# Optimization experiments

Hardware: AMD Instinct MI355X
Metric: run time of the kernel (lower is better)

The kernel has to match this reference:

```python
import jax, jax.numpy as jnp
import numpy as np

B, H, L, DK = 16, 16, 2048, 64   # batch, heads, query len, head dim
LK = 4096                        # original key length
C = 10                           # num_clusters
LKS = 2 * int(np.log(LK))        # shrunk key length = 16


def _lin(x, w, b):
    # torch nn.Linear: y = x @ W^T + b
    return jnp.matmul(x, w.T) + b


def setup_inputs() -> dict:
    key = jax.random.key(0)
    ks = jax.random.split(key, 20)
    s = 0.05
    inp = {
        "Q": jax.random.normal(ks[0], (B, H, L, DK), jnp.float32),
        "K": jax.random.normal(ks[1], (B, H, LK, DK), jnp.float32),
        "V": jax.random.normal(ks[2], (B, H, LK, DK), jnp.float32),
        # shrink_k / shrink_v: Linear(l_k, 2*log(l_k))
        "shrink_k_w": jax.random.normal(ks[3], (LKS, LK), jnp.float32) * s,
        "shrink_k_b": jax.random.normal(ks[4], (LKS,), jnp.float32) * s,
        "shrink_v_w": jax.random.normal(ks[5], (LKS, LK), jnp.float32) * s,
        "shrink_v_b": jax.random.normal(ks[6], (LKS,), jnp.float32) * s,
        # proj_to_cluster_k: Linear(batch_size, num_clusters) + ReLU
        "proj_w": jax.random.normal(ks[7], (C, B), jnp.float32) * s,
        "proj_b": jax.random.normal(ks[8], (C,), jnp.float32) * s,
        "ck_w": jax.random.normal(ks[9], (C, C), jnp.float32) * s,
        "ck_b": jax.random.normal(ks[10], (C,), jnp.float32) * s,
        "cq_w": jax.random.normal(ks[11], (C, C), jnp.float32) * s,
        "cq_b": jax.random.normal(ks[12], (C,), jnp.float32) * s,
        "mu_w": jax.random.normal(ks[13], (C, C), jnp.float32) * s,
        "mu_b": jax.random.normal(ks[14], (C,), jnp.float32) * s,
        "sig_w": jax.random.normal(ks[15], (C, C), jnp.float32) * s,
        "sig_b": jax.random.normal(ks[16], (C,), jnp.float32) * s,
    }
    return inp


def reference(Q, K, V, shrink_k_w, shrink_k_b, shrink_v_w, shrink_v_b,
              proj_w, proj_b, ck_w, ck_b, cq_w, cq_b, mu_w, mu_b, sig_w, sig_b):
    b = Q.shape[0]
    # shrink along key sequence dim: (b,h,lk,d) -> (b,h,LKS,d)
    Ks = jnp.einsum('bhkd,sk->bhsd', K, shrink_k_w) + shrink_k_b[:, None]
    Vs = jnp.einsum('bhkd,sk->bhsd', V, shrink_v_w) + shrink_v_b[:, None]

    # pad + unfold over the batch dim: window j of K_padded[w:w+b]
    K_padded = jnp.concatenate([jnp.zeros_like(Ks), Ks[1:]], axis=0)  # (2b-1,h,LKS,d)
    idx = jnp.arange(b)[:, None] + jnp.arange(b)[None, :]             # (b, b)
    K_unfold = jnp.moveaxis(K_padded[idx], 1, -1)                     # (b,h,LKS,d,b)

    cluster_k_p = jax.nn.relu(_lin(K_unfold, proj_w, proj_b))         # (b,h,LKS,d,C)
    cluster_k = jax.nn.softmax(_lin(cluster_k_p, ck_w, ck_b), axis=-1)
    cluster_q = jax.nn.softmax(_lin(cluster_k_p, cq_w, cq_b), axis=-1)

    mu = _lin(cluster_q, mu_w, mu_b)
    sigma = jax.nn.softplus(_lin(cluster_q, sig_w, sig_b))
    # Normal log_prob
    log_prob = (-0.5 * jnp.square((cluster_k - mu) / sigma)
                - jnp.log(sigma) - 0.5 * jnp.log(2.0 * jnp.pi).astype(cluster_k.dtype))
    # torch CrossEntropyLoss with probability targets: class dim = dim 1 (= h)
    logp = jax.nn.log_softmax(cluster_q, axis=1)
    ce = -jnp.mean(jnp.sum(cluster_q * logp, axis=1))
    loss = -jnp.mean(log_prob) + ce

    # per-cluster masked mean over the last dim, vectorized over clusters.
    # where(argmax==i, cluster_q, 0).mean(-1) == onehot(argmax)[...,i] * mean(cluster_q,-1)
    masks = jax.nn.one_hot(jnp.argmax(cluster_q, axis=-1), C, dtype=cluster_q.dtype)  # (b,h,LKS,d,C)
    q_mean = jnp.mean(cluster_q, axis=-1)                                              # (b,h,LKS,d)
    q_sub = masks * q_mean[..., None]                                                  # (b,h,LKS,d,C)

    scores = jnp.einsum('bhqd,bhkdc->cbhqk', Q, q_sub)  # (C,b,h,l,LKS)
    final_score = jnp.max(scores, axis=0)               # (b,h,l,LKS)
    attn = jax.nn.softmax(final_score, axis=-1)
    context = jnp.einsum('bhqk,bhkd->bhqd', attn, Vs)   # (b,h,l,d)
    return context, loss
```

## Files before the change

### kernel.cpp

```cpp
#include <hip/hip_runtime.h>

#define KS_OFF 0
#define VS_OFF 262144
#define QM_OFF 524288
#define AM_OFF 786432
#define LP_OFF 1048576
#define CE_OFF 1048832

typedef __attribute__((ext_vector_type(8))) short short8;
typedef __attribute__((ext_vector_type(4))) float f32x4;

__device__ inline unsigned short bfb(float x) {
  unsigned u = __float_as_uint(x);
  return (unsigned short)((u + 0x7fffu + ((u >> 16) & 1u)) >> 16);
}
__device__ inline unsigned pk2(float a, float b) {
  return (unsigned)bfb(a) | ((unsigned)bfb(b) << 16);
}
__device__ inline float bft(unsigned short h) {
  return __uint_as_float((unsigned)h << 16);
}
__device__ inline void split3(float x, unsigned short& h, unsigned short& m, unsigned short& l) {
  unsigned u = __float_as_uint(x);
  h = (unsigned short)(u >> 16);
  float r = x - bft(h);
  m = (unsigned short)(__float_as_uint(r) >> 16);
  float r2 = r - bft(m);
  l = bfb(r2);
}

__global__ __launch_bounds__(256) void k_shrink3(
    const float* __restrict__ K, const float* __restrict__ V,
    const float* __restrict__ skw, const float* __restrict__ skb,
    const float* __restrict__ svw, const float* __restrict__ svb,
    float* __restrict__ ws)
{
  int blk = blockIdx.x;
  int tensor = blk >> 8;
  int bh = blk & 255;
  const float* __restrict__ src = (tensor ? V : K) + (size_t)bh * (4096 * 64);
  const float* __restrict__ w    = tensor ? svw : skw;
  const float* __restrict__ bias = tensor ? svb : skb;
  float* __restrict__ dst = ws + (tensor ? VS_OFF : KS_OFF) + bh * 1024;

  int t = threadIdx.x;
  int wv = t >> 6;
  int l = t & 63;
  int l15 = l & 15;
  int kg = l >> 4;
  union Frag { unsigned u[4]; short8 s8; };

  f32x4 acc[4];
#pragma unroll
  for (int nt = 0; nt < 4; ++nt) acc[nt] = (f32x4){0.f, 0.f, 0.f, 0.f};

  const float* __restrict__ wrow = w + l15 * 4096 + kg * 8;

  int kk0 = wv * 32;
  for (int kk = kk0; kk < kk0 + 32; ++kk) {
    const float* __restrict__ wp = wrow + kk * 32;
    float4 wa = *(const float4*)wp;
    float4 wb = *(const float4*)(wp + 4);
    float we[8] = {wa.x, wa.y, wa.z, wa.w, wb.x, wb.y, wb.z, wb.w};
    Frag ah, am, al;
#pragma unroll
    for (int e = 0; e < 4; ++e) {
      unsigned short h0, m0, l0, h1, m1, l1;
      split3(we[2 * e], h0, m0, l0);
      split3(we[2 * e + 1], h1, m1, l1);
      ah.u[e] = (unsigned)h0 | ((unsigned)h1 << 16);
      am.u[e] = (unsigned)m0 | ((unsigned)m1 << 16);
      al.u[e] = (unsigned)l0 | ((unsigned)l1 << 16);
    }

    int kbase = kk * 32 + kg * 8;
    const float* __restrict__ bp = src + (size_t)kbase * 64 + l15;
#pragma unroll
    for (int nt = 0; nt < 4; ++nt) {
      float v[8];
#pragma unroll
      for (int j = 0; j < 8; ++j) v[j] = bp[j * 64 + nt * 16];
      Frag bh, bm, bl;
#pragma unroll
      for (int e = 0; e < 4; ++e) {
        unsigned short h0, m0, l0, h1, m1, l1;
        split3(v[2 * e], h0, m0, l0);
        split3(v[2 * e + 1], h1, m1, l1);
        bh.u[e] = (unsigned)h0 | ((unsigned)h1 << 16);
        bm.u[e] = (unsigned)m0 | ((unsigned)m1 << 16);
        bl.u[e] = (unsigned)l0 | ((unsigned)l1 << 16);
      }
      acc[nt] = __builtin_amdgcn_mfma_f32_16x16x32_bf16(ah.s8, bh.s8, acc[nt], 0, 0, 0);
      acc[nt] = __builtin_amdgcn_mfma_f32_16x16x32_bf16(ah.s8, bm.s8, acc[nt], 0, 0, 0);
      acc[nt] = __builtin_amdgcn_mfma_f32_16x16x32_bf16(am.s8, bh.s8, acc[nt], 0, 0, 0);
      acc[nt] = __builtin_amdgcn_mfma_f32_16x16x32_bf16(ah.s8, bl.s8, acc[nt], 0, 0, 0);
      acc[nt] = __builtin_amdgcn_mfma_f32_16x16x32_bf16(al.s8, bh.s8, acc[nt], 0, 0, 0);
      acc[nt] = __builtin_amdgcn_mfma_f32_16x16x32_bf16(am.s8, bm.s8, acc[nt], 0, 0, 0);
    }
  }

  __shared__ float red[4][1024];
  int g4 = kg * 4;
#pragma unroll
  for (int nt = 0; nt < 4; ++nt)
#pragma unroll
    for (int r = 0; r < 4; ++r)
      red[wv][(g4 + r) * 64 + nt * 16 + l15] = acc[nt][r];
  __syncthreads();
  for (int p = t; p < 1024; p += 256) {
    int s = p >> 6;
    dst[p] = red[0][p] + red[1][p] + red[2][p] + red[3][p] + bias[s];
  }
}

__global__ __launch_bounds__(1024) void k_cluster(
    const float* __restrict__ pw, const float* __restrict__ pb,
    const float* __restrict__ ckw, const float* __restrict__ ckb,
    const float* __restrict__ cqw, const float* __restrict__ cqb,
    const float* __restrict__ muw, const float* __restrict__ mub,
    const float* __restrict__ sgw, const float* __restrict__ sgb,
    float* __restrict__ ws)
{
  int bidx = blockIdx.x >> 4;
  int sIdx = blockIdx.x & 15;
  int t = threadIdx.x;
  int h = t >> 6, d = t & 63;

  __shared__ float wgt[610];
  __shared__ float cqs[16 * 64 * 10];
  if (t < 160) wgt[t] = pw[t];
  else if (t < 170) wgt[t] = pb[t - 160];
  else if (t < 270) wgt[t] = ckw[t - 170];
  else if (t < 280) wgt[t] = ckb[t - 270];
  else if (t < 380) wgt[t] = cqw[t - 280];
  else if (t < 390) wgt[t] = cqb[t - 380];
  else if (t < 490) wgt[t] = muw[t - 390];
  else if (t < 500) wgt[t] = mub[t - 490];
  else if (t < 600) wgt[t] = sgw[t - 500];
  else if (t < 610) wgt[t] = sgb[t - 600];
  __syncthreads();

  const float* __restrict__ Ks = ws + KS_OFF;

  float ckp[10];
#pragma unroll
  for (int c = 0; c < 10; ++c) ckp[c] = wgt[160 + c];
  for (int m = 1; m <= bidx; ++m) {
    float kv = Ks[((m * 16 + h) * 16 + sIdx) * 64 + d];
    int j = m + 15 - bidx;
#pragma unroll
    for (int c = 0; c < 10; ++c) ckp[c] = fmaf(kv, wgt[c * 16 + j], ckp[c]);
  }
#pragma unroll
  for (int c = 0; c < 10; ++c) ckp[c] = fmaxf(ckp[c], 0.f);

  float zk[10], zq[10];
#pragma unroll
  for (int c = 0; c < 10; ++c) { zk[c] = wgt[270 + c]; zq[c] = wgt[380 + c]; }
#pragma unroll
  for (int j = 0; j < 10; ++j) {
    float v = ckp[j];
#pragma unroll
    for (int c = 0; c < 10; ++c) {
      zk[c] = fmaf(v, wgt[170 + c * 10 + j], zk[c]);
      zq[c] = fmaf(v, wgt[280 + c * 10 + j], zq[c]);
    }
  }
  float mk = zk[0], mq = zq[0];
#pragma unroll
  for (int c = 1; c < 10; ++c) { mk = fmaxf(mk, zk[c]); mq = fmaxf(mq, zq[c]); }
  float sk = 0.f, sq = 0.f;
#pragma unroll
  for (int c = 0; c < 10; ++c) {
    zk[c] = expf(zk[c] - mk); sk += zk[c];
    zq[c] = expf(zq[c] - mq); sq += zq[c];
  }
  float rik = 1.f / sk, riq = 1.f / sq;
#pragma unroll
  for (int c = 0; c < 10; ++c) { zk[c] *= rik; zq[c] *= riq; }

  float mu[10], sgz[10];
#pragma unroll
  for (int c = 0; c < 10; ++c) { mu[c] = wgt[490 + c]; sgz[c] = wgt[600 + c]; }
#pragma unroll
  for (int j = 0; j < 10; ++j) {
    float v = zq[j];
#pragma unroll
    for (int c = 0; c < 10; ++c) {
      mu[c]  = fmaf(v, wgt[390 + c * 10 + j], mu[c]);
      sgz[c] = fmaf(v, wgt[500 + c * 10 + j], sgz[c]);
    }
  }
  float lp = 0.f, qmean = 0.f, best = zq[0];
  int amax = 0;
#pragma unroll
  for (int c = 0; c < 10; ++c) {
    float x = sgz[c];
    float sg = (x > 20.f) ? x : log1pf(expf(x));
    float zr = (zk[c] - mu[c]) / sg;
    lp += -0.5f * zr * zr - logf(sg);
    qmean += zq[c];
    if (c > 0 && zq[c] > best) { best = zq[c]; amax = c; }
  }
  lp -= 10.f * 0.91893853320467274f;
  qmean *= 0.1f;

  int pos = ((bidx * 16 + h) * 16 + sIdx) * 64 + d;
  ws[QM_OFF + pos] = qmean;
  ((int*)ws)[AM_OFF + pos] = amax;
#pragma unroll
  for (int c = 0; c < 10; ++c) cqs[(h * 64 + d) * 10 + c] = zq[c];
  __syncthreads();

  float ce = 0.f;
  if (t < 640) {
    int dd = t / 10, cc = t - dd * 10;
    float x[16];
#pragma unroll
    for (int hh = 0; hh < 16; ++hh) x[hh] = cqs[(hh * 64 + dd) * 10 + cc];
    float mx = x[0];
#pragma unroll
    for (int hh = 1; hh < 16; ++hh) mx = fmaxf(mx, x[hh]);
    float sum = 0.f;
#pragma unroll
    for (int hh = 0; hh < 16; ++hh) sum += expf(x[hh] - mx);
    float lse = mx + logf(sum);
#pragma unroll
    for (int hh = 0; hh < 16; ++hh) ce += x[hh] * (x[hh] - lse);
  }

#pragma unroll
  for (int o = 1; o < 64; o <<= 1) { lp += __shfl_xor(lp, o); ce += __shfl_xor(ce, o); }
  __shared__ float redw[16][2];
  if ((t & 63) == 0) { redw[t >> 6][0] = lp; redw[t >> 6][1] = ce; }
  __syncthreads();
  if (t == 0) {
    float Ls = 0.f, Cs = 0.f;
#pragma unroll
    for (int i = 0; i < 16; ++i) { Ls += redw[i][0]; Cs += redw[i][1]; }
    ws[LP_OFF + blockIdx.x] = Ls;
    ws[CE_OFF + blockIdx.x] = Cs;
  }
}

__global__ __launch_bounds__(512, 4) void k_attn(
    const float* __restrict__ Q, float* __restrict__ out,
    const float* __restrict__ ws)
{
  int bid = blockIdx.x;
  int bh = bid >> 1;
  int half = bid & 1;
  int t = threadIdx.x;
  int wv = t >> 6;
  int l = t & 63;
  int l15 = l & 15;
  int sbase = (l >> 4) * 8;
  int g4 = (l >> 4) * 4;

  __shared__ unsigned short Gm[10][16][72];
  __shared__ float Vs_l[1024];
  __shared__ unsigned short attn_l[8][16][32];

  const float* __restrict__ qmp = ws + QM_OFF + bh * 1024;
  const int* __restrict__ amp = (const int*)ws + AM_OFF + bh * 1024;
  const float* __restrict__ vsp = ws + VS_OFF + bh * 1024;

  for (int i = t; i < 5760; i += 512) ((unsigned*)Gm)[i] = 0u;
  for (int i = t; i < 2048; i += 512) ((unsigned*)attn_l)[i] = 0u;
  for (int i = t; i < 1024; i += 512) Vs_l[i] = vsp[i];
  __syncthreads();
  for (int p = t; p < 1024; p += 512) {
    int s = p >> 6, dd = p & 63;
    Gm[amp[p]][s][dd] = bfb(qmp[p]);
  }
  __syncthreads();

  union Frag { unsigned u[4]; short8 s8; };

  Frag vf[4];
#pragma unroll
  for (int dt = 0; dt < 4; ++dt) {
#pragma unroll
    for (int e2 = 0; e2 < 4; ++e2) {
      int s0 = sbase + e2 * 2;
      float a = (s0 < 16) ? Vs_l[s0 * 64 + dt * 16 + l15] : 0.f;
      float b = (s0 + 1 < 16) ? Vs_l[(s0 + 1) * 64 + dt * 16 + l15] : 0.f;
      vf[dt].u[e2] = pk2(a, b);
    }
  }

  for (int tt = 0; tt < 8; ++tt) {
    int qbase = half * 1024 + wv * 128 + tt * 16;
    const float* __restrict__ qptr = Q + ((size_t)bh * 2048 + qbase) * 64 + l15 * 64;

    Frag bf[2];
#pragma unroll
    for (int ks = 0; ks < 2; ++ks) {
      const float* p = qptr + sbase + ks * 32;
      float4 a = *(const float4*)p;
      float4 b2 = *(const float4*)(p + 4);
      bf[ks].u[0] = pk2(a.x, a.y);
      bf[ks].u[1] = pk2(a.z, a.w);
      bf[ks].u[2] = pk2(b2.x, b2.y);
      bf[ks].u[3] = pk2(b2.z, b2.w);
    }

    f32x4 acc[10];
#pragma unroll
    for (int c = 0; c < 10; ++c) acc[c] = (f32x4){0.f, 0.f, 0.f, 0.f};
#pragma unroll
    for (int ks = 0; ks < 2; ++ks) {
#pragma unroll
      for (int c = 0; c < 10; ++c) {
        short8 af = *(const short8*)(const void*)&Gm[c][l15][sbase + ks * 32];
        acc[c] = __builtin_amdgcn_mfma_f32_16x16x32_bf16(af, bf[ks].s8, acc[c], 0, 0, 0);
      }
    }
    f32x4 fs = acc[0];
#pragma unroll
    for (int c = 1; c < 10; ++c) {
      fs.x = fmaxf(fs.x, acc[c].x); fs.y = fmaxf(fs.y, acc[c].y);
      fs.z = fmaxf(fs.z, acc[c].z); fs.w = fmaxf(fs.w, acc[c].w);
    }
    float mx = fmaxf(fmaxf(fs.x, fs.y), fmaxf(fs.z, fs.w));
    mx = fmaxf(mx, __shfl_xor(mx, 16));
    mx = fmaxf(mx, __shfl_xor(mx, 32));
    float e0 = __expf(fs.x - mx), e1 = __expf(fs.y - mx),
          e2 = __expf(fs.z - mx), e3 = __expf(fs.w - mx);
    float ssum = e0 + e1 + e2 + e3;
    ssum += __shfl_xor(ssum, 16);
    ssum += __shfl_xor(ssum, 32);
    float inv = 1.f / ssum;
    unsigned* awp = (unsigned*)&attn_l[wv][l15][g4];
    awp[0] = pk2(e0 * inv, e1 * inv);
    awp[1] = pk2(e2 * inv, e3 * inv);
    short8 b2f = *(const short8*)(const void*)&attn_l[wv][l15][sbase];
#pragma unroll
    for (int dt = 0; dt < 4; ++dt) {
      f32x4 ct = (f32x4){0.f, 0.f, 0.f, 0.f};
      ct = __builtin_amdgcn_mfma_f32_16x16x32_bf16(vf[dt].s8, b2f, ct, 0, 0, 0);
      float* op = out + ((size_t)bh * 2048 + qbase + l15) * 64 + dt * 16 + g4;
      *(f32x4*)op = ct;
    }
  }

  if (bid == 0 && t == 0) {
    float Ls = 0.f, Cs = 0.f;
    for (int i = 0; i < 256; ++i) { Ls += ws[LP_OFF + i]; Cs += ws[CE_OFF + i]; }
    out[33554432] = -Ls / 2621440.f - Cs / 163840.f;
  }
}

extern "C" void kernel_launch(void* const* d_in, const int* in_sizes, int n_in,
                              void* d_out, int out_size, void* d_ws, size_t ws_size,
                              hipStream_t stream) {
  const float* Q   = (const float*)d_in[0];
  const float* K   = (const float*)d_in[1];
  const float* V   = (const float*)d_in[2];
  const float* skw = (const float*)d_in[3];
  const float* skb = (const float*)d_in[4];
  const float* svw = (const float*)d_in[5];
  const float* svb = (const float*)d_in[6];
  const float* pw  = (const float*)d_in[7];
  const float* pb  = (const float*)d_in[8];
  const float* ckw = (const float*)d_in[9];
  const float* ckb = (const float*)d_in[10];
  const float* cqw = (const float*)d_in[11];
  const float* cqb = (const float*)d_in[12];
  const float* muw = (const float*)d_in[13];
  const float* mub = (const float*)d_in[14];
  const float* sgw = (const float*)d_in[15];
  const float* sgb = (const float*)d_in[16];
  float* out = (float*)d_out;
  float* ws  = (float*)d_ws;

  hipLaunchKernelGGL(k_shrink3, dim3(512), dim3(256), 0, stream, K, V, skw, skb, svw, svb, ws);
  hipLaunchKernelGGL(k_cluster, dim3(256), dim3(1024), 0, stream,
                     pw, pb, ckw, ckb, cqw, cqb, muw, mub, sgw, sgb, ws);
  hipLaunchKernelGGL(k_attn, dim3(512), dim3(512), 0, stream, Q, out, ws);
}
```

Before: 329.2 us.

## Split shrink reduction across more blocks and widen attention grid

The key/value shrink kernel is split four ways along the key dimension: each block writes a partial sum into the output buffer used as scratch, and a new reduction kernel adds the partials and the bias. The attention kernel now gives each block one eighth of the queries instead of one half, with four times as many blocks and a lower occupancy hint. Both changes aim to fill the GPU better on the memory-bound shrink and the attention phase. The cost is an extra launch, partial-sum traffic through global memory, and redundant per-block setup (cluster matrix build and Vs load) repeated four times as often in attention.

```diff
diff --git a/kernel.cpp b/kernel.cpp
--- a/kernel.cpp
+++ b/kernel.cpp
@@ -29,19 +29,18 @@
   l = bfb(r2);
 }
 
-__global__ __launch_bounds__(256) void k_shrink3(
+__global__ __launch_bounds__(256) void k_shrink4(
     const float* __restrict__ K, const float* __restrict__ V,
-    const float* __restrict__ skw, const float* __restrict__ skb,
-    const float* __restrict__ svw, const float* __restrict__ svb,
-    float* __restrict__ ws)
+    const float* __restrict__ skw, const float* __restrict__ svw,
+    float* __restrict__ part)
 {
   int blk = blockIdx.x;
-  int tensor = blk >> 8;
-  int bh = blk & 255;
+  int q = blk & 3;
+  int bh = (blk >> 2) & 255;
+  int tensor = blk >> 10;
   const float* __restrict__ src = (tensor ? V : K) + (size_t)bh * (4096 * 64);
-  const float* __restrict__ w    = tensor ? svw : skw;
-  const float* __restrict__ bias = tensor ? svb : skb;
-  float* __restrict__ dst = ws + (tensor ? VS_OFF : KS_OFF) + bh * 1024;
+  const float* __restrict__ w   = tensor ? svw : skw;
+  float* __restrict__ dst = part + (size_t)blk * 1024;
 
   int t = threadIdx.x;
   int wv = t >> 6;
@@ -56,8 +55,8 @@
 
   const float* __restrict__ wrow = w + l15 * 4096 + kg * 8;
 
-  int kk0 = wv * 32;
-  for (int kk = kk0; kk < kk0 + 32; ++kk) {
+  int kk0 = q * 32 + wv * 8;
+  for (int kk = kk0; kk < kk0 + 8; ++kk) {
     const float* __restrict__ wp = wrow + kk * 32;
     float4 wa = *(const float4*)wp;
     float4 wb = *(const float4*)(wp + 4);
@@ -107,10 +106,22 @@
     for (int r = 0; r < 4; ++r)
       red[wv][(g4 + r) * 64 + nt * 16 + l15] = acc[nt][r];
   __syncthreads();
-  for (int p = t; p < 1024; p += 256) {
-    int s = p >> 6;
-    dst[p] = red[0][p] + red[1][p] + red[2][p] + red[3][p] + bias[s];
-  }
+  for (int p = t; p < 1024; p += 256)
+    dst[p] = red[0][p] + red[1][p] + red[2][p] + red[3][p];
+}
+
+__global__ __launch_bounds__(256) void k_shrink_red(
+    const float* __restrict__ part, const float* __restrict__ skb,
+    const float* __restrict__ svb, float* __restrict__ ws)
+{
+  int blk = blockIdx.x;
+  int tensor = blk >> 8;
+  int bh = blk & 255;
+  const float* __restrict__ p0 = part + ((size_t)(tensor * 1024 + bh * 4)) * 1024;
+  const float* __restrict__ bias = tensor ? svb : skb;
+  float* __restrict__ dst = ws + (tensor ? VS_OFF : KS_OFF) + bh * 1024;
+  for (int p = threadIdx.x; p < 1024; p += 256)
+    dst[p] = ((p0[p] + p0[1024 + p]) + (p0[2048 + p] + p0[3072 + p])) + bias[p >> 6];
 }
 
 __global__ __launch_bounds__(1024) void k_cluster(
@@ -243,13 +254,13 @@
   }
 }
 
-__global__ __launch_bounds__(512, 4) void k_attn(
+__global__ __launch_bounds__(512, 2) void k_attn(
     const float* __restrict__ Q, float* __restrict__ out,
     const float* __restrict__ ws)
 {
   int bid = blockIdx.x;
-  int bh = bid >> 1;
-  int half = bid & 1;
+  int bh = bid >> 3;
+  int eighth = bid & 7;
   int t = threadIdx.x;
   int wv = t >> 6;
   int l = t & 63;
@@ -289,8 +300,8 @@
     }
   }
 
-  for (int tt = 0; tt < 8; ++tt) {
-    int qbase = half * 1024 + wv * 128 + tt * 16;
+  for (int tt = 0; tt < 2; ++tt) {
+    int qbase = eighth * 256 + wv * 32 + tt * 16;
     const float* __restrict__ qptr = Q + ((size_t)bh * 2048 + qbase) * 64 + l15 * 64;
 
     Frag bf[2];
@@ -374,8 +385,9 @@
   float* out = (float*)d_out;
   float* ws  = (float*)d_ws;
 
-  hipLaunchKernelGGL(k_shrink3, dim3(512), dim3(256), 0, stream, K, V, skw, skb, svw, svb, ws);
+  hipLaunchKernelGGL(k_shrink4, dim3(2048), dim3(256), 0, stream, K, V, skw, svw, out);
+  hipLaunchKernelGGL(k_shrink_red, dim3(512), dim3(256), 0, stream, out, skb, svb, ws);
   hipLaunchKernelGGL(k_cluster, dim3(256), dim3(1024), 0, stream,
                      pw, pb, ckw, ckb, cqw, cqb, muw, mub, sgw, sgb, ws);
-  hipLaunchKernelGGL(k_attn, dim3(512), dim3(512), 0, stream, Q, out, ws);
-}
+  hipLaunchKernelGGL(k_attn, dim3(2048), dim3(512), 0, stream, Q, out, ws);
+}
```

Result: faster. 308.8 us (-6.2%).
